# Kernel tuning notes

Measured on AMD Instinct MI355X. Metric: run time of the kernel, lower is better.

Reference implementation:

```python
import jax, jax.numpy as jnp
import numpy as np

B, S, H = 1, 1024, 2880
NQ, NKV, D = 64, 8, 64          # query heads, kv heads, head_dim
G = NQ // NKV                    # GQA group size
W = 128                          # sliding window
SCALE = D ** -0.5
NEG = -1e30


def rotate_half(x):
    x1, x2 = jnp.split(x, 2, axis=-1)
    return jnp.concatenate((-x2, x1), axis=-1)


def setup_inputs() -> dict:
    key = jax.random.key(0)
    ks = jax.random.split(key, 8)
    hidden_states = jax.random.normal(ks[0], (B, S, H), jnp.float32)
    # rotary tables, half head_dim (module concats (cos,cos) to full dim)
    pos = jnp.arange(S, dtype=jnp.float32)[:, None]
    inv = 1.0 / (10000.0 ** (jnp.arange(0, D, 2, dtype=jnp.float32) / D))
    ang = pos * inv[None, :]                      # (S, D/2)
    cos = jnp.cos(ang)[None].astype(jnp.float32)  # (1, S, D/2)
    sin = jnp.sin(ang)[None].astype(jnp.float32)
    w_qkv = jax.random.normal(ks[1], (H, (NQ + 2 * NKV) * D), jnp.float32) * 0.02
    b_qkv = jax.random.normal(ks[2], ((NQ + 2 * NKV) * D,), jnp.float32) * 0.02
    w_o = jax.random.normal(ks[3], (NQ * D, H), jnp.float32) * 0.02
    b_o = jax.random.normal(ks[4], (H,), jnp.float32) * 0.02
    sinks = jax.random.normal(ks[5], (NQ,), jnp.float32)
    k_cache = jnp.zeros((B, S, NKV, D), jnp.float32)
    v_cache = jnp.zeros((B, S, NKV, D), jnp.float32)
    return {"hidden_states": hidden_states, "cos": cos, "sin": sin,
            "w_qkv": w_qkv, "b_qkv": b_qkv, "w_o": w_o, "b_o": b_o,
            "sinks": sinks, "k_cache": k_cache, "v_cache": v_cache, "kv_len": 0}


def reference(hidden_states, cos, sin, w_qkv, b_qkv, w_o, b_o, sinks,
              k_cache, v_cache, kv_len):
    # fused QKV projection + split
    qkv = hidden_states @ w_qkv + b_qkv                      # (B, S, (NQ+2*NKV)*D)
    q, k, v = jnp.split(qkv, [NQ * D, NQ * D + NKV * D], axis=-1)
    q = q.reshape(B, S, NQ, D)
    k = k.reshape(B, S, NKV, D)
    v = v.reshape(B, S, NKV, D)
    # RoPE (BSND layout, half-dim tables duplicated to full dim)
    cosf = jnp.concatenate((cos, cos), axis=-1)[:, :, None, :]
    sinf = jnp.concatenate((sin, sin), axis=-1)[:, :, None, :]
    q = q * cosf + rotate_half(q) * sinf
    k = k * cosf + rotate_half(k) * sinf
    # KV-cache scatter update at position kv_len along seq dim
    k_cache = jax.lax.dynamic_update_slice(k_cache, k, (0, kv_len, 0, 0))
    v_cache = jax.lax.dynamic_update_slice(v_cache, v, (0, kv_len, 0, 0))
    T = kv_len + S
    keys = k_cache[:, :T]                                    # (B, T, NKV, D)
    vals = v_cache[:, :T]
    # GQA: group query heads by kv head
    qg = q.reshape(B, S, NKV, G, D)
    scores = jnp.einsum('bqhgd,bkhd->bhgqk', qg, keys) * SCALE  # (B,NKV,G,S,T)
    # causal + sliding-window mask
    i = jnp.arange(S)[:, None] + kv_len
    j = jnp.arange(T)[None, :]
    allowed = (j <= i) & (i - j < W)
    scores = jnp.where(allowed, scores, NEG)
    # softmax with per-head learnable sink logit (sink gets no value)
    sk = sinks.reshape(NKV, G)[None, :, :, None]             # (1,NKV,G,1)
    m = jnp.maximum(jnp.max(scores, axis=-1), sk)            # (B,NKV,G,S)
    p = jnp.exp(scores - m[..., None])
    denom = jnp.sum(p, axis=-1) + jnp.exp(sk - m)
    attn = jnp.einsum('bhgqk,bkhd->bqhgd', p / denom[..., None], vals)
    out = attn.reshape(B, S, NQ * D) @ w_o + b_o             # (B, S, H)
    return out
```

## Files before the change

### kernel.cpp

```cpp
#include <hip/hip_runtime.h>
#include <hip/hip_bf16.h>

#define NQH 64
#define NKVH 8
#define DH 64
#define SEQ 1024
#define HID 2880
#define QKV_N 5120
#define ATTN_N 4096
#define WIN 128
#define WO_NPAD 2880
#define SCALE_F 0.125f

typedef __attribute__((ext_vector_type(8))) __bf16 bf16x8;
typedef __attribute__((ext_vector_type(4))) float f32x4;

#define GLOAD_LDS16(g, l) \
    __builtin_amdgcn_global_load_lds((const __attribute__((address_space(1))) void*)(g), \
                                     (__attribute__((address_space(3))) void*)(l), 16, 0, 0)

__device__ __forceinline__ ushort f2bf(float x) {
    union { float f; unsigned int u; } c; c.f = x;
    unsigned int u = c.u;
    unsigned int r = (u + 0x7FFFu + ((u >> 16) & 1u)) >> 16;
    return (ushort)r;
}

__global__ __launch_bounds__(256) void convert_f32_bf16(
    const float* __restrict__ in, ushort* __restrict__ out, int n4)
{
    int idx = blockIdx.x * blockDim.x + threadIdx.x;
    int stride = gridDim.x * blockDim.x;
    for (int i = idx; i < n4; i += stride) {
        float4 v = reinterpret_cast<const float4*>(in)[i];
        ushort4 o;
        o.x = f2bf(v.x); o.y = f2bf(v.y); o.z = f2bf(v.z); o.w = f2bf(v.w);
        reinterpret_cast<ushort4*>(out)[i] = o;
    }
}

__global__ __launch_bounds__(256) void transpose_convert(
    const float* __restrict__ in, ushort* __restrict__ out, int K, int N)
{
    __shared__ ushort tile[64][80];
    const int bk = blockIdx.x * 64;
    const int bn = blockIdx.y * 64;
    const int tid = threadIdx.x;
    const bool inb = bn < N;

#pragma unroll
    for (int it = 0; it < 4; ++it) {
        int r = it * 16 + (tid >> 4);
        int c4 = (tid & 15) * 4;
        float4 v = make_float4(0.f, 0.f, 0.f, 0.f);
        if (inb) v = *(const float4*)&in[(size_t)(bk + r) * N + bn + c4];
        tile[c4 + 0][r] = f2bf(v.x);
        tile[c4 + 1][r] = f2bf(v.y);
        tile[c4 + 2][r] = f2bf(v.z);
        tile[c4 + 3][r] = f2bf(v.w);
    }
    __syncthreads();
#pragma unroll
    for (int it = 0; it < 2; ++it) {
        int nr = it * 32 + (tid >> 3);
        int c8 = (tid & 7) * 8;
        uint4 v = *(const uint4*)&tile[nr][c8];
        *(uint4*)&out[(size_t)(bn + nr) * K + bk + c8] = v;
    }
}

template<int BM, int BN, int WAVES_N>
__global__ __launch_bounds__(512) void gemm_bal(
    const ushort* __restrict__ A, const ushort* __restrict__ BT,
    const float* __restrict__ bias, float* __restrict__ C,
    int K, int ldC, int Nreal)
{
    constexpr int WAVES_M = 8 / WAVES_N;
    constexpr int WM = BM / WAVES_M;
    constexpr int WN = BN / WAVES_N;
    constexpr int MR = WM / 16;
    constexpr int NR = WN / 16;
    constexpr int ASZ = BM * 64;
    constexpr int BSZ = BN * 64;
    constexpr int ACH = BM * 8;
    constexpr int TOTCH = (BM + BN) * 8;
    constexpr int NLOAD = (TOTCH + 511) / 512;

    __shared__ ushort Al[2 * ASZ];
    __shared__ ushort Bl[2 * BSZ];

    const int t = threadIdx.x;
    const int lane = t & 63;
    const int w = t >> 6;
    const int wr = w / WAVES_N;
    const int wc = w % WAVES_N;
    const int g4 = lane >> 4;
    const int r15 = lane & 15;

    const int nx = gridDim.x;
    const int flat = blockIdx.x + nx * blockIdx.y;
    const int per = (nx * gridDim.y) >> 3;
    const int virt = (flat & 7) * per + (flat >> 3);
    const int n0 = (virt % nx) * BN;
    const int m0 = (virt / nx) * BM;

    const ushort* src[NLOAD];
    ushort* d0[NLOAD];
    ushort* d1[NLOAD];
#pragma unroll
    for (int i = 0; i < NLOAD; ++i) {
        int lin = i * 512 + t;
        src[i] = nullptr; d0[i] = nullptr; d1[i] = nullptr;
        if (lin < ACH) {
            int row = lin >> 3, ch = (lin & 7) ^ (row & 7);
            src[i] = A + (size_t)(m0 + row) * K + ch * 8;
            d0[i] = &Al[lin * 8];
            d1[i] = &Al[ASZ + lin * 8];
        } else if (lin < TOTCH) {
            int l2 = lin - ACH;
            int row = l2 >> 3, ch = (l2 & 7) ^ (row & 7);
            src[i] = BT + (size_t)(n0 + row) * K + ch * 8;
            d0[i] = &Bl[l2 * 8];
            d1[i] = &Bl[BSZ + l2 * 8];
        }
    }

#define STAGE_TILE(buf) do { \
        _Pragma("unroll") \
        for (int i = 0; i < NLOAD; ++i) \
            if (src[i]) { \
                GLOAD_LDS16(src[i], (buf) ? d1[i] : d0[i]); \
                src[i] += 64; \
            } \
    } while (0)

    int aoff[MR][2], boff[NR][2];
#pragma unroll
    for (int mi = 0; mi < MR; ++mi)
#pragma unroll
        for (int ks = 0; ks < 2; ++ks) {
            int row = wr * WM + mi * 16 + r15;
            aoff[mi][ks] = row * 64 + (((ks * 4 + g4) ^ (row & 7)) * 8);
        }
#pragma unroll
    for (int ni = 0; ni < NR; ++ni)
#pragma unroll
        for (int ks = 0; ks < 2; ++ks) {
            int col = wc * WN + ni * 16 + r15;
            boff[ni][ks] = col * 64 + (((ks * 4 + g4) ^ (col & 7)) * 8);
        }

    f32x4 acc[MR][NR];
#pragma unroll
    for (int mi = 0; mi < MR; ++mi)
#pragma unroll
        for (int ni = 0; ni < NR; ++ni) acc[mi][ni] = (f32x4){0.f, 0.f, 0.f, 0.f};

#define COMPUTE_TILE(buf) do { \
        const ushort* Ab = &Al[(buf) * ASZ]; \
        const ushort* Bb = &Bl[(buf) * BSZ]; \
        _Pragma("unroll") \
        for (int ks = 0; ks < 2; ++ks) { \
            bf16x8 af[MR], bfr[NR]; \
            _Pragma("unroll") \
            for (int mi = 0; mi < MR; ++mi) af[mi] = *(const bf16x8*)&Ab[aoff[mi][ks]]; \
            _Pragma("unroll") \
            for (int ni = 0; ni < NR; ++ni) bfr[ni] = *(const bf16x8*)&Bb[boff[ni][ks]]; \
            _Pragma("unroll") \
            for (int mi = 0; mi < MR; ++mi) \
                _Pragma("unroll") \
                for (int ni = 0; ni < NR; ++ni) \
                    acc[mi][ni] = __builtin_amdgcn_mfma_f32_16x16x32_bf16(af[mi], bfr[ni], acc[mi][ni], 0, 0, 0); \
        } \
    } while (0)

    const int NT = K >> 6;
    STAGE_TILE(0);
    __syncthreads();
    for (int kt = 0; kt < NT; kt += 2) {
        if (kt + 1 < NT) STAGE_TILE(1);
        COMPUTE_TILE(0);
        __syncthreads();
        if (kt + 1 < NT) {
            if (kt + 2 < NT) STAGE_TILE(0);
            COMPUTE_TILE(1);
            __syncthreads();
        }
    }
#undef STAGE_TILE
#undef COMPUTE_TILE

#pragma unroll
    for (int ni = 0; ni < NR; ++ni) {
        int col = n0 + wc * WN + ni * 16 + r15;
        if (col < Nreal) {
            float bv = bias[col];
#pragma unroll
            for (int mi = 0; mi < MR; ++mi) {
                int row = m0 + wr * WM + mi * 16 + g4 * 4;
#pragma unroll
                for (int r = 0; r < 4; ++r)
                    C[(size_t)(row + r) * ldC + col] = acc[mi][ni][r] + bv;
            }
        }
    }
}

__global__ __launch_bounds__(512) void attn_mfma_kernel(
    const float* __restrict__ qkv, const float* __restrict__ sinks,
    const float* __restrict__ cosp, const float* __restrict__ sinp,
    ushort* __restrict__ attn_out)
{
    __shared__ __align__(16) ushort Kl[160][72];
    __shared__ __align__(16) ushort Vt[64][168];
    __shared__ __align__(16) ushort Pl[8][32][40];
    const int t = threadIdx.x;
    const int w = t >> 6;
    const int l = t & 63;
    const int g4 = l >> 4;
    const int r15 = l & 15;
    const int q0 = blockIdx.x * 32;
    const int hk = blockIdx.y;
    const int kbase = q0 - 128;

#pragma unroll
    for (int i = 0; i < 5; ++i) {
        int idx = i * 512 + t;
        int row = idx >> 4;
        int c4 = (idx & 15) * 4;
        int j = kbase + row;
        float4 kr = make_float4(0.f, 0.f, 0.f, 0.f);
        float4 vv = make_float4(0.f, 0.f, 0.f, 0.f);
        if (j >= 0) {
            const float* kb = &qkv[(size_t)j * QKV_N + 4096 + hk * 64];
            float4 kx = *(const float4*)&kb[c4];
            float4 ky = *(const float4*)&kb[c4 ^ 32];
            float4 cs = *(const float4*)&cosp[j * 32 + (c4 & 31)];
            float4 sn = *(const float4*)&sinp[j * 32 + (c4 & 31)];
            if (c4 < 32) {
                kr.x = kx.x * cs.x - ky.x * sn.x; kr.y = kx.y * cs.y - ky.y * sn.y;
                kr.z = kx.z * cs.z - ky.z * sn.z; kr.w = kx.w * cs.w - ky.w * sn.w;
            } else {
                kr.x = kx.x * cs.x + ky.x * sn.x; kr.y = kx.y * cs.y + ky.y * sn.y;
                kr.z = kx.z * cs.z + ky.z * sn.z; kr.w = kx.w * cs.w + ky.w * sn.w;
            }
            vv = *(const float4*)&qkv[(size_t)j * QKV_N + 4608 + hk * 64 + c4];
        }
        ushort4 kp;
        kp.x = f2bf(kr.x); kp.y = f2bf(kr.y); kp.z = f2bf(kr.z); kp.w = f2bf(kr.w);
        *(ushort4*)&Kl[row][c4] = kp;
        Vt[c4 + 0][row] = f2bf(vv.x);
        Vt[c4 + 1][row] = f2bf(vv.y);
        Vt[c4 + 2][row] = f2bf(vv.z);
        Vt[c4 + 3][row] = f2bf(vv.w);
    }

    bf16x8 qf[2][2];
#pragma unroll
    for (int ct = 0; ct < 2; ++ct) {
        int R = w * 32 + ct * 16 + r15;
        int q = q0 + (R & 31);
        int hq = hk * 8 + (R >> 5);
        const float* qb = &qkv[(size_t)q * QKV_N + hq * 64];
        int d8 = g4 * 8;
        float4 a0 = *(const float4*)&qb[d8];
        float4 b0 = *(const float4*)&qb[d8 + 4];
        float4 a1 = *(const float4*)&qb[32 + d8];
        float4 b1 = *(const float4*)&qb[32 + d8 + 4];
        float4 c0 = *(const float4*)&cosp[q * 32 + d8];
        float4 c1 = *(const float4*)&cosp[q * 32 + d8 + 4];
        float4 s0 = *(const float4*)&sinp[q * 32 + d8];
        float4 s1 = *(const float4*)&sinp[q * 32 + d8 + 4];
        union { ushort u[8]; bf16x8 v; } p0, p1;
        p0.u[0] = f2bf((a0.x * c0.x - a1.x * s0.x) * SCALE_F);
        p0.u[1] = f2bf((a0.y * c0.y - a1.y * s0.y) * SCALE_F);
        p0.u[2] = f2bf((a0.z * c0.z - a1.z * s0.z) * SCALE_F);
        p0.u[3] = f2bf((a0.w * c0.w - a1.w * s0.w) * SCALE_F);
        p0.u[4] = f2bf((b0.x * c1.x - b1.x * s1.x) * SCALE_F);
        p0.u[5] = f2bf((b0.y * c1.y - b1.y * s1.y) * SCALE_F);
        p0.u[6] = f2bf((b0.z * c1.z - b1.z * s1.z) * SCALE_F);
        p0.u[7] = f2bf((b0.w * c1.w - b1.w * s1.w) * SCALE_F);
        p1.u[0] = f2bf((a1.x * c0.x + a0.x * s0.x) * SCALE_F);
        p1.u[1] = f2bf((a1.y * c0.y + a0.y * s0.y) * SCALE_F);
        p1.u[2] = f2bf((a1.z * c0.z + a0.z * s0.z) * SCALE_F);
        p1.u[3] = f2bf((a1.w * c0.w + a0.w * s0.w) * SCALE_F);
        p1.u[4] = f2bf((b1.x * c1.x + b0.x * s1.x) * SCALE_F);
        p1.u[5] = f2bf((b1.y * c1.y + b0.y * s1.y) * SCALE_F);
        p1.u[6] = f2bf((b1.z * c1.z + b0.z * s1.z) * SCALE_F);
        p1.u[7] = f2bf((b1.w * c1.w + b0.w * s1.w) * SCALE_F);
        qf[ct][0] = p0.v;
        qf[ct][1] = p1.v;
    }
    __syncthreads();

    f32x4 sc[10][2];
#pragma unroll
    for (int kt = 0; kt < 10; ++kt) {
        sc[kt][0] = (f32x4){0.f, 0.f, 0.f, 0.f};
        sc[kt][1] = (f32x4){0.f, 0.f, 0.f, 0.f};
    }
#pragma unroll
    for (int kt = 0; kt < 10; ++kt) {
#pragma unroll
        for (int s = 0; s < 2; ++s) {
            bf16x8 kf = *(const bf16x8*)&Kl[kt * 16 + r15][s * 32 + g4 * 8];
            sc[kt][0] = __builtin_amdgcn_mfma_f32_16x16x32_bf16(kf, qf[0][s], sc[kt][0], 0, 0, 0);
            sc[kt][1] = __builtin_amdgcn_mfma_f32_16x16x32_bf16(kf, qf[1][s], sc[kt][1], 0, 0, 0);
        }
    }

    const int minkey = 128 - q0;
#pragma unroll
    for (int ct = 0; ct < 2; ++ct) {
        int R = w * 32 + ct * 16 + r15;
        int ql = R & 31;
        float snk = sinks[hk * 8 + (R >> 5)];
#pragma unroll
        for (int kt = 0; kt < 10; ++kt)
#pragma unroll
            for (int r = 0; r < 4; ++r) {
                int key = kt * 16 + g4 * 4 + r;
                bool ok = (key > ql) && (key <= ql + 128) && (key >= minkey);
                if (!ok) sc[kt][ct][r] = -1e30f;
            }
        float m = snk;
#pragma unroll
        for (int kt = 0; kt < 10; ++kt)
#pragma unroll
            for (int r = 0; r < 4; ++r) m = fmaxf(m, sc[kt][ct][r]);
        m = fmaxf(m, __shfl_xor(m, 16));
        m = fmaxf(m, __shfl_xor(m, 32));
        float sum = 0.f;
#pragma unroll
        for (int kt = 0; kt < 10; ++kt)
#pragma unroll
            for (int r = 0; r < 4; ++r) {
                float p = __expf(sc[kt][ct][r] - m);
                sc[kt][ct][r] = p;
                sum += p;
            }
        sum += __shfl_xor(sum, 16);
        sum += __shfl_xor(sum, 32);
        sum += __expf(snk - m);
        float iv = 1.0f / sum;
#pragma unroll
        for (int kt = 0; kt < 10; ++kt)
#pragma unroll
            for (int r = 0; r < 4; ++r) sc[kt][ct][r] *= iv;
    }

    f32x4 pv[2][4];
#pragma unroll
    for (int mi = 0; mi < 2; ++mi)
#pragma unroll
        for (int ni = 0; ni < 4; ++ni) pv[mi][ni] = (f32x4){0.f, 0.f, 0.f, 0.f};

#pragma unroll
    for (int s = 0; s < 5; ++s) {
#pragma unroll
        for (int ct = 0; ct < 2; ++ct)
#pragma unroll
            for (int kh = 0; kh < 2; ++kh) {
                int kt = 2 * s + kh;
                ushort4 p4;
                p4.x = f2bf(sc[kt][ct][0]);
                p4.y = f2bf(sc[kt][ct][1]);
                p4.z = f2bf(sc[kt][ct][2]);
                p4.w = f2bf(sc[kt][ct][3]);
                *(ushort4*)&Pl[w][ct * 16 + r15][kh * 16 + g4 * 4] = p4;
            }
#pragma unroll
        for (int mi = 0; mi < 2; ++mi) {
            bf16x8 pf = *(const bf16x8*)&Pl[w][mi * 16 + r15][g4 * 8];
#pragma unroll
            for (int ni = 0; ni < 4; ++ni) {
                bf16x8 vf = *(const bf16x8*)&Vt[ni * 16 + r15][s * 32 + g4 * 8];
                pv[mi][ni] = __builtin_amdgcn_mfma_f32_16x16x32_bf16(pf, vf, pv[mi][ni], 0, 0, 0);
            }
        }
    }

#pragma unroll
    for (int mi = 0; mi < 2; ++mi)
#pragma unroll
        for (int r = 0; r < 4; ++r) {
            int R = w * 32 + mi * 16 + g4 * 4 + r;
            int q = q0 + (R & 31);
            int hq = hk * 8 + (R >> 5);
            ushort* ob = &attn_out[(size_t)q * ATTN_N + hq * 64 + r15];
#pragma unroll
            for (int ni = 0; ni < 4; ++ni)
                ob[ni * 16] = f2bf(pv[mi][ni][r]);
        }
}

extern "C" void kernel_launch(void* const* d_in, const int* in_sizes, int n_in,
                              void* d_out, int out_size, void* d_ws, size_t ws_size,
                              hipStream_t stream)
{
    const float* hidden = (const float*)d_in[0];
    const float* cosp   = (const float*)d_in[1];
    const float* sinp   = (const float*)d_in[2];
    const float* w_qkv  = (const float*)d_in[3];
    const float* b_qkv  = (const float*)d_in[4];
    const float* w_o    = (const float*)d_in[5];
    const float* b_o    = (const float*)d_in[6];
    const float* sinks  = (const float*)d_in[7];

    char* ws = (char*)d_ws;
    size_t off = 0;
    ushort* wqkvT = (ushort*)(ws + off); off += (size_t)QKV_N * HID * 2;
    ushort* woT   = (ushort*)(ws + off); off += (size_t)WO_NPAD * ATTN_N * 2;
    float*  qkv   = (float*)(ws + off);  off += (size_t)SEQ * QKV_N * 4;
    ushort* hidden_b = (ushort*)(ws + off);
    ushort* attn_b   = (ushort*)(ws + off); off += (size_t)SEQ * ATTN_N * 2;
    if (off > ws_size) return;

    transpose_convert<<<dim3(HID / 64, QKV_N / 64), 256, 0, stream>>>(w_qkv, wqkvT, HID, QKV_N);
    transpose_convert<<<dim3(ATTN_N / 64, WO_NPAD / 64), 256, 0, stream>>>(w_o, woT, ATTN_N, HID);
    convert_f32_bf16<<<2048, 256, 0, stream>>>(hidden, hidden_b, SEQ * HID / 4);

    gemm_bal<128, 160, 2><<<dim3(QKV_N / 160, SEQ / 128), 512, 0, stream>>>(
        hidden_b, wqkvT, b_qkv, qkv, HID, QKV_N, QKV_N);

    attn_mfma_kernel<<<dim3(SEQ / 32, NKVH), 512, 0, stream>>>(
        qkv, sinks, cosp, sinp, attn_b);

    gemm_bal<128, 96, 2><<<dim3(HID / 96, SEQ / 128), 512, 0, stream>>>(
        attn_b, woT, b_o, (float*)d_out, ATTN_N, HID, HID);
}
```

Measured before the change: 152.3 us.

## Switch GEMMs to 32x32x16 bf16 MFMA with retuned tile shapes

Replaces the 16x16x32 MFMA tiles in both projection GEMMs with 32x32x16 MFMA, which changes the per-lane LDS fragment offsets, the 16-register accumulator and the epilogue row mapping. The QKV GEMM tile moves from 128x160 to 128x128 and the output GEMM tile from 128x96 to 128x64, adjusting grid sizes to match. The larger MFMA shape is meant to raise math throughput per LDS read. The trade-off is more accumulator registers and a different grid and occupancy balance.

```diff
diff --git a/kernel.cpp b/kernel.cpp
--- a/kernel.cpp
+++ b/kernel.cpp
@@ -14,6 +14,7 @@
 
 typedef __attribute__((ext_vector_type(8))) __bf16 bf16x8;
 typedef __attribute__((ext_vector_type(4))) float f32x4;
+typedef __attribute__((ext_vector_type(16))) float f32x16;
 
 #define GLOAD_LDS16(g, l) \
     __builtin_amdgcn_global_load_lds((const __attribute__((address_space(1))) void*)(g), \
@@ -70,7 +71,7 @@
 }
 
 template<int BM, int BN, int WAVES_N>
-__global__ __launch_bounds__(512) void gemm_bal(
+__global__ __launch_bounds__(512) void gemm32(
     const ushort* __restrict__ A, const ushort* __restrict__ BT,
     const float* __restrict__ bias, float* __restrict__ C,
     int K, int ldC, int Nreal)
@@ -78,8 +79,8 @@
     constexpr int WAVES_M = 8 / WAVES_N;
     constexpr int WM = BM / WAVES_M;
     constexpr int WN = BN / WAVES_N;
-    constexpr int MR = WM / 16;
-    constexpr int NR = WN / 16;
+    constexpr int MR = WM / 32;
+    constexpr int NR = WN / 32;
     constexpr int ASZ = BM * 64;
     constexpr int BSZ = BN * 64;
     constexpr int ACH = BM * 8;
@@ -94,8 +95,8 @@
     const int w = t >> 6;
     const int wr = w / WAVES_N;
     const int wc = w % WAVES_N;
-    const int g4 = lane >> 4;
-    const int r15 = lane & 15;
+    const int l31 = lane & 31;
+    const int lh = lane >> 5;
 
     const int nx = gridDim.x;
     const int flat = blockIdx.x + nx * blockIdx.y;
@@ -134,33 +135,35 @@
             } \
     } while (0)
 
-    int aoff[MR][2], boff[NR][2];
+    int aoff[MR][4], boff[NR][4];
 #pragma unroll
     for (int mi = 0; mi < MR; ++mi)
 #pragma unroll
-        for (int ks = 0; ks < 2; ++ks) {
-            int row = wr * WM + mi * 16 + r15;
-            aoff[mi][ks] = row * 64 + (((ks * 4 + g4) ^ (row & 7)) * 8);
+        for (int ks = 0; ks < 4; ++ks) {
+            int row = wr * WM + mi * 32 + l31;
+            aoff[mi][ks] = row * 64 + (((ks * 2 + lh) ^ (row & 7)) * 8);
         }
 #pragma unroll
     for (int ni = 0; ni < NR; ++ni)
 #pragma unroll
-        for (int ks = 0; ks < 2; ++ks) {
-            int col = wc * WN + ni * 16 + r15;
-            boff[ni][ks] = col * 64 + (((ks * 4 + g4) ^ (col & 7)) * 8);
-        }
-
-    f32x4 acc[MR][NR];
+        for (int ks = 0; ks < 4; ++ks) {
+            int col = wc * WN + ni * 32 + l31;
+            boff[ni][ks] = col * 64 + (((ks * 2 + lh) ^ (col & 7)) * 8);
+        }
+
+    f32x16 acc[MR][NR];
 #pragma unroll
     for (int mi = 0; mi < MR; ++mi)
 #pragma unroll
-        for (int ni = 0; ni < NR; ++ni) acc[mi][ni] = (f32x4){0.f, 0.f, 0.f, 0.f};
+        for (int ni = 0; ni < NR; ++ni)
+#pragma unroll
+            for (int r = 0; r < 16; ++r) acc[mi][ni][r] = 0.f;
 
 #define COMPUTE_TILE(buf) do { \
         const ushort* Ab = &Al[(buf) * ASZ]; \
         const ushort* Bb = &Bl[(buf) * BSZ]; \
         _Pragma("unroll") \
-        for (int ks = 0; ks < 2; ++ks) { \
+        for (int ks = 0; ks < 4; ++ks) { \
             bf16x8 af[MR], bfr[NR]; \
             _Pragma("unroll") \
             for (int mi = 0; mi < MR; ++mi) af[mi] = *(const bf16x8*)&Ab[aoff[mi][ks]]; \
@@ -170,7 +173,7 @@
             for (int mi = 0; mi < MR; ++mi) \
                 _Pragma("unroll") \
                 for (int ni = 0; ni < NR; ++ni) \
-                    acc[mi][ni] = __builtin_amdgcn_mfma_f32_16x16x32_bf16(af[mi], bfr[ni], acc[mi][ni], 0, 0, 0); \
+                    acc[mi][ni] = __builtin_amdgcn_mfma_f32_32x32x16_bf16(af[mi], bfr[ni], acc[mi][ni], 0, 0, 0); \
         } \
     } while (0)
 
@@ -192,15 +195,17 @@
 
 #pragma unroll
     for (int ni = 0; ni < NR; ++ni) {
-        int col = n0 + wc * WN + ni * 16 + r15;
+        int col = n0 + wc * WN + ni * 32 + l31;
         if (col < Nreal) {
             float bv = bias[col];
 #pragma unroll
             for (int mi = 0; mi < MR; ++mi) {
-                int row = m0 + wr * WM + mi * 16 + g4 * 4;
-#pragma unroll
-                for (int r = 0; r < 4; ++r)
-                    C[(size_t)(row + r) * ldC + col] = acc[mi][ni][r] + bv;
+                int rbase = m0 + wr * WM + mi * 32 + 4 * lh;
+#pragma unroll
+                for (int reg = 0; reg < 16; ++reg) {
+                    int row = rbase + (reg & 3) + 8 * (reg >> 2);
+                    C[(size_t)row * ldC + col] = acc[mi][ni][reg] + bv;
+                }
             }
         }
     }
@@ -420,12 +425,12 @@
     transpose_convert<<<dim3(ATTN_N / 64, WO_NPAD / 64), 256, 0, stream>>>(w_o, woT, ATTN_N, HID);
     convert_f32_bf16<<<2048, 256, 0, stream>>>(hidden, hidden_b, SEQ * HID / 4);
 
-    gemm_bal<128, 160, 2><<<dim3(QKV_N / 160, SEQ / 128), 512, 0, stream>>>(
+    gemm32<128, 128, 2><<<dim3(QKV_N / 128, SEQ / 128), 512, 0, stream>>>(
         hidden_b, wqkvT, b_qkv, qkv, HID, QKV_N, QKV_N);
 
     attn_mfma_kernel<<<dim3(SEQ / 32, NKVH), 512, 0, stream>>>(
         qkv, sinks, cosp, sinp, attn_b);
 
-    gemm_bal<128, 96, 2><<<dim3(HID / 96, SEQ / 128), 512, 0, stream>>>(
+    gemm32<128, 64, 2><<<dim3(HID / 64, SEQ / 128), 512, 0, stream>>>(
         attn_b, woT, b_o, (float*)d_out, ATTN_N, HID, HID);
 }
```

After: 150.4 us. Within noise of the previous version (-1.2%).
